# Optimization experiments

Hardware: AMD Instinct MI355X
Metric: run time of the kernel (lower is better)

## Reference

```python
import jax, jax.numpy as jnp
import numpy as np

N_NODES = 100000
N_EDGES = 3200000
DIM = 64


def setup_inputs() -> dict:
    key = jax.random.key(0)
    k1, k2, k3, k4, k5, k6 = jax.random.split(key, 6)
    lap_rows = jax.random.randint(k1, (N_EDGES,), 0, N_NODES, dtype=jnp.int32)
    lap_cols = jax.random.randint(k2, (N_EDGES,), 0, N_NODES, dtype=jnp.int32)
    # normalized-Laplacian-like positive values
    lap_vals = jax.random.uniform(k3, (N_EDGES,), dtype=jnp.float32) * 0.1
    features = jax.random.normal(k4, (N_NODES, DIM), dtype=jnp.float32)
    scale = 1.0 / np.sqrt(DIM)
    W1 = jax.random.normal(k5, (DIM, DIM), dtype=jnp.float32) * scale
    b1 = jnp.zeros((DIM,), dtype=jnp.float32)
    W2 = jax.random.normal(k6, (DIM, DIM), dtype=jnp.float32) * scale
    b2 = jnp.zeros((DIM,), dtype=jnp.float32)
    return {
        "lap_rows": lap_rows, "lap_cols": lap_cols, "lap_vals": lap_vals,
        "features": features, "W1": W1, "b1": b1, "W2": W2, "b2": b2,
    }


def reference(lap_rows, lap_cols, lap_vals, features, W1, b1, W2, b2):
    # x = L @ features  (COO SpMM: gather source rows, scale, scatter-add to dest)
    msgs = lap_vals[:, None] * features[lap_cols]            # [E, D]
    x = jax.ops.segment_sum(msgs, lap_rows, num_segments=N_NODES)  # [N, D]
    # output = (L+I) E W1 + (L E * E) W2
    inter_part1 = (features + x) @ W1 + b1                   # [N, D_out]
    inter_part2 = (x * features) @ W2 + b2                   # [N, D_out]
    return inter_part1 + inter_part2
```

## Files before the change

### kernel.cpp

```cpp
#include <hip/hip_runtime.h>
#include <hip/hip_fp16.h>

#define DIM 64
#define RPB 128
#define RPB_SHIFT 7
#define SUP_SHIFT 11
#define SB_MAX 64
#define HTILE_H 16384
#define HTILE1 4096
#define HTILE2 4096
#define XSCALE 4194304.0f
#define XINV   2.384185791015625e-7f

typedef _Float16 half8 __attribute__((ext_vector_type(8)));
typedef float    f32x4 __attribute__((ext_vector_type(4)));
typedef float    f32x2 __attribute__((ext_vector_type(2)));

template <bool HI>
__device__ __forceinline__ f32x2 q2f(unsigned int w)
{
    return __builtin_amdgcn_cvt_pk_f32_fp8(w, HI);
}

__global__ __launch_bounds__(256) void scatter_kernel(
    const int* __restrict__ rows, const int* __restrict__ cols,
    const float* __restrict__ vals, const float* __restrict__ feat,
    float* __restrict__ x, int E)
{
    unsigned long long t = (unsigned long long)blockIdx.x * blockDim.x + threadIdx.x;
    int e = (int)(t >> 6);
    int d = (int)(t & 63);
    if (e >= E) return;
    int r = rows[e];
    int c = cols[e];
    float v = vals[e];
    float f = feat[(size_t)c * DIM + d];
    atomicAdd(&x[(size_t)r * DIM + d], v * f);
}

__global__ __launch_bounds__(256) void cvt_kernel(
    const float* __restrict__ f, __half* __restrict__ h, int n2)
{
    int i = blockIdx.x * blockDim.x + threadIdx.x;
    if (i < n2) {
        float2 v = ((const float2*)f)[i];
        __half2 o;
        o.x = __float2half(v.x);
        o.y = __float2half(v.y);
        ((__half2*)h)[i] = o;
    }
}

__global__ __launch_bounds__(1024) void prep_kernel(
    const float* __restrict__ feat, __half* __restrict__ featH,
    unsigned char* __restrict__ featQ,
    const int* __restrict__ rows, int* __restrict__ gcnt,
    int n8, int NC, int E, int B)
{
    if ((int)blockIdx.x < NC) {
        int i = blockIdx.x * 1024 + threadIdx.x;
        if (i < n8) {
            const float4* src = (const float4*)(feat + (size_t)i * 8);
            float4 a = src[0], b = src[1];
            __half2 h0 = __floats2half2_rn(a.x, a.y);
            __half2 h1 = __floats2half2_rn(a.z, a.w);
            __half2 h2 = __floats2half2_rn(b.x, b.y);
            __half2 h3 = __floats2half2_rn(b.z, b.w);
            float4 ho;
            ho.x = __builtin_bit_cast(float, h0);
            ho.y = __builtin_bit_cast(float, h1);
            ho.z = __builtin_bit_cast(float, h2);
            ho.w = __builtin_bit_cast(float, h3);
            *(float4*)(featH + (size_t)i * 8) = ho;
            unsigned int q0 = __builtin_amdgcn_cvt_pk_fp8_f32(a.x, a.y, 0, false);
            q0 = __builtin_amdgcn_cvt_pk_fp8_f32(a.z, a.w, (int)q0, true);
            unsigned int q1 = __builtin_amdgcn_cvt_pk_fp8_f32(b.x, b.y, 0, false);
            q1 = __builtin_amdgcn_cvt_pk_fp8_f32(b.z, b.w, (int)q1, true);
            uint2 qo; qo.x = q0; qo.y = q1;
            *(uint2*)(featQ + (size_t)i * 8) = qo;
        }
    } else {
        extern __shared__ int lcnt[];
        for (int i = threadIdx.x; i < B; i += 1024) lcnt[i] = 0;
        __syncthreads();
        int base = ((int)blockIdx.x - NC) * HTILE_H;
#pragma unroll
        for (int k = 0; k < HTILE_H / 1024; ++k) {
            int e = base + k * 1024 + threadIdx.x;
            if (e < E) atomicAdd(&lcnt[rows[e] >> RPB_SHIFT], 1);
        }
        __syncthreads();
        for (int i = threadIdx.x; i < B; i += 1024)
            if (lcnt[i]) atomicAdd(&gcnt[i], lcnt[i]);
    }
}

__global__ __launch_bounds__(1024) void scan_kernel(
    const int* __restrict__ gcnt, int* __restrict__ offs, int* __restrict__ cursors,
    int* __restrict__ soffs, int* __restrict__ scursors, int B, int SB, int E)
{
    __shared__ int lds[2048];
    int t = threadIdx.x;
    int c0 = (t < B) ? gcnt[t] : 0;
    int c1 = (t + 1024 < B) ? gcnt[t + 1024] : 0;
    lds[t] = c0;
    lds[t + 1024] = c1;
    __syncthreads();
    for (int off = 1; off < 2048; off <<= 1) {
        int a = (t >= off) ? lds[t - off] : 0;
        int b = lds[t + 1024 - off];
        __syncthreads();
        lds[t] += a;
        lds[t + 1024] += b;
        __syncthreads();
    }
    if (t < B) {
        int e = lds[t] - c0;
        offs[t] = e; cursors[t] = e;
        if ((t & 15) == 0) { soffs[t >> 4] = e; scursors[t >> 4] = e; }
    }
    int t2 = t + 1024;
    if (t2 < B) {
        int e = lds[t2] - c1;
        offs[t2] = e; cursors[t2] = e;
        if ((t2 & 15) == 0) { soffs[t2 >> 4] = e; scursors[t2 >> 4] = e; }
    }
    if (t == 0) { offs[B] = E; soffs[SB] = E; }
}

__global__ __launch_bounds__(1024) void superbin_kernel(
    const int* __restrict__ rows, const int* __restrict__ cols,
    const float* __restrict__ vals, int* __restrict__ scursors,
    unsigned long long* __restrict__ sorted1, int E, int SB)
{
    __shared__ int cnt[SB_MAX];
    __shared__ int bse[SB_MAX];
    const int tid = threadIdx.x;
    if (tid < SB) cnt[tid] = 0;
    __syncthreads();
    const int tbase = blockIdx.x * HTILE1;
    int rr[HTILE1 / 1024];
#pragma unroll
    for (int k = 0; k < HTILE1 / 1024; ++k) {
        int e = tbase + k * 1024 + tid;
        rr[k] = (e < E) ? rows[e] : -1;
        if (rr[k] >= 0) atomicAdd(&cnt[rr[k] >> SUP_SHIFT], 1);
    }
    __syncthreads();
    if (tid < SB) {
        int c = cnt[tid];
        bse[tid] = c ? atomicAdd(&scursors[tid], c) : 0;
        cnt[tid] = 0;
    }
    __syncthreads();
#pragma unroll
    for (int k = 0; k < HTILE1 / 1024; ++k) {
        int e = tbase + k * 1024 + tid;
        if (rr[k] >= 0) {
            int r  = rr[k];
            int sb = r >> SUP_SHIFT;
            int slot = bse[sb] + atomicAdd(&cnt[sb], 1);
            unsigned long long pk =
                ((unsigned long long)__float_as_uint(vals[e]) << 32) |
                ((unsigned long long)(r & 2047) << 17) |
                (unsigned)cols[e];
            sorted1[slot] = pk;
        }
    }
}

__global__ __launch_bounds__(1024) void finebin_kernel(
    const unsigned long long* __restrict__ sorted1, const int* __restrict__ soffs,
    int* __restrict__ cursors, unsigned long long* __restrict__ sorted2,
    int E, int B, int SB)
{
    extern __shared__ int l[];
    int* cnt  = l;
    int* bse  = l + B;
    int* sofl = l + 2 * B;
    const int tid = threadIdx.x;
    if (tid <= SB) sofl[tid] = soffs[tid];
    for (int i = tid; i < B; i += 1024) cnt[i] = 0;
    __syncthreads();

    const int tbase = blockIdx.x * HTILE2;
    int sb0 = 0;
    {
        int lo = 0, hi = SB - 1;
        while (lo < hi) {
            int mid = (lo + hi + 1) >> 1;
            if (sofl[mid] <= tbase) lo = mid; else hi = mid - 1;
        }
        sb0 = lo;
    }

    unsigned long long pkr[HTILE2 / 1024];
    int fidr[HTILE2 / 1024];
#pragma unroll
    for (int k = 0; k < HTILE2 / 1024; ++k) {
        int i = tbase + k * 1024 + tid;
        if (i < E) {
            pkr[k] = sorted1[i];
            int sb = sb0;
            while (sofl[sb + 1] <= i) sb++;
            fidr[k] = (sb << 4) + (int)((pkr[k] >> 24) & 15);
            atomicAdd(&cnt[fidr[k]], 1);
        } else fidr[k] = -1;
    }
    __syncthreads();
    for (int i = tid; i < B; i += 1024) {
        int c = cnt[i];
        bse[i] = c ? atomicAdd(&cursors[i], c) : 0;
    }
    __syncthreads();
    for (int i = tid; i < B; i += 1024) cnt[i] = 0;
    __syncthreads();
#pragma unroll
    for (int k = 0; k < HTILE2 / 1024; ++k) {
        if (fidr[k] >= 0) {
            int f = fidr[k];
            int slot = bse[f] + atomicAdd(&cnt[f], 1);
            sorted2[slot] = pkr[k];
        }
    }
}

__global__ __launch_bounds__(1024, 4) void reduce_fused_mfma_kernel(
    const unsigned long long* __restrict__ sorted, const int* __restrict__ offs,
    const unsigned char* __restrict__ featQ, const __half* __restrict__ featH,
    const float* __restrict__ W1, const float* __restrict__ b1,
    const float* __restrict__ W2, const float* __restrict__ b2,
    float* __restrict__ out, int N)
{
    __shared__ int   xi[RPB][DIM + 4];
    __shared__ half8 Wl[1024];
    __shared__ float biasl[DIM];

    const int tid = threadIdx.x;
    const int b   = blockIdx.x;

    {
        int t    = tid >> 8;
        int c    = (tid >> 6) & 3;
        int quad = (tid >> 4) & 3;
        int m    = tid & 15;
        const float* Wsrc = (t < 2) ? W1 : W2;
        int kbase = (t & 1) * 32 + quad * 8;
        int col   = c * 16 + m;
        half8 wv;
#pragma unroll
        for (int j = 0; j < 8; ++j)
            wv[j] = (_Float16)Wsrc[(kbase + j) * DIM + col];
        Wl[tid] = wv;
        if (tid < DIM) biasl[tid] = b1[tid] + b2[tid];
    }
    for (int i = tid; i < RPB * (DIM + 4); i += 1024) ((int*)xi)[i] = 0;
    __syncthreads();

    const int s = offs[b], t = offs[b + 1];
    const int grp = tid >> 3;
    const int sub = tid & 7;
    const int rowbase = b * RPB;

#define EDGE_ACC(PK, Q)                                                      \
    {                                                                        \
        int   rl = (int)(((PK) >> 17) & (RPB - 1));                          \
        float v  = __uint_as_float((unsigned)((PK) >> 32)) * XSCALE;         \
        int* base = &xi[rl][sub * 8];                                        \
        f32x2 f0 = q2f<false>((Q).x);                                        \
        f32x2 f1 = q2f<true >((Q).x);                                        \
        f32x2 f2 = q2f<false>((Q).y);                                        \
        f32x2 f3 = q2f<true >((Q).y);                                        \
        atomicAdd(base + 0, (int)(f0[0] * v));                               \
        atomicAdd(base + 1, (int)(f0[1] * v));                               \
        atomicAdd(base + 2, (int)(f1[0] * v));                               \
        atomicAdd(base + 3, (int)(f1[1] * v));                               \
        atomicAdd(base + 4, (int)(f2[0] * v));                               \
        atomicAdd(base + 5, (int)(f2[1] * v));                               \
        atomicAdd(base + 6, (int)(f3[0] * v));                               \
        atomicAdd(base + 7, (int)(f3[1] * v));                               \
    }

    int i = s + grp;
    for (; i + 384 < t; i += 512) {
        unsigned long long pk0 = sorted[i];
        unsigned long long pk1 = sorted[i + 128];
        unsigned long long pk2 = sorted[i + 256];
        unsigned long long pk3 = sorted[i + 384];
        uint2 q0 = *(const uint2*)(featQ + ((size_t)(pk0 & 0x1FFFFu) << 6) + sub * 8);
        uint2 q1 = *(const uint2*)(featQ + ((size_t)(pk1 & 0x1FFFFu) << 6) + sub * 8);
        uint2 q2 = *(const uint2*)(featQ + ((size_t)(pk2 & 0x1FFFFu) << 6) + sub * 8);
        uint2 q3 = *(const uint2*)(featQ + ((size_t)(pk3 & 0x1FFFFu) << 6) + sub * 8);
        EDGE_ACC(pk0, q0)
        EDGE_ACC(pk1, q1)
        EDGE_ACC(pk2, q2)
        EDGE_ACC(pk3, q3)
    }
    for (; i < t; i += 128) {
        unsigned long long pk0 = sorted[i];
        uint2 q0 = *(const uint2*)(featQ + ((size_t)(pk0 & 0x1FFFFu) << 6) + sub * 8);
        EDGE_ACC(pk0, q0)
    }
#undef EDGE_ACC
    __syncthreads();

    const int w    = tid >> 6;
    const int lane = tid & 63;
    const int m    = lane & 15;
    const int quad = lane >> 4;

#pragma unroll
    for (int it = 0; it < 2; ++it) {
        int task = w + 16 * it;
        int tile = task >> 2;
        int cw   = task & 3;

        const int fb = cw * 64 + quad * 16 + m;
        half8 wf0 = Wl[fb];
        half8 wf1 = Wl[fb + 256];
        half8 wf2 = Wl[fb + 512];
        half8 wf3 = Wl[fb + 768];
        float bias = biasl[cw * 16 + m];

        int rowl = tile * 16 + m;
        int grow = rowbase + rowl;
        int rldr = (grow < N) ? grow : (N - 1);
        const __half* fp = featH + (size_t)rldr * DIM + quad * 8;
        half8 flo = *(const half8*)(fp);
        half8 fhi = *(const half8*)(fp + 32);
        const int* xp = &xi[rowl][quad * 8];
        int4 xl0 = *(const int4*)(xp);
        int4 xl1 = *(const int4*)(xp + 4);
        int4 xh0 = *(const int4*)(xp + 32);
        int4 xh1 = *(const int4*)(xp + 36);

        half8 alo, ahi, blo, bhi;
        _Float16 xv;
        xv = (_Float16)((float)xl0.x * XINV); alo[0] = flo[0] + xv; blo[0] = flo[0] * xv;
        xv = (_Float16)((float)xl0.y * XINV); alo[1] = flo[1] + xv; blo[1] = flo[1] * xv;
        xv = (_Float16)((float)xl0.z * XINV); alo[2] = flo[2] + xv; blo[2] = flo[2] * xv;
        xv = (_Float16)((float)xl0.w * XINV); alo[3] = flo[3] + xv; blo[3] = flo[3] * xv;
        xv = (_Float16)((float)xl1.x * XINV); alo[4] = flo[4] + xv; blo[4] = flo[4] * xv;
        xv = (_Float16)((float)xl1.y * XINV); alo[5] = flo[5] + xv; blo[5] = flo[5] * xv;
        xv = (_Float16)((float)xl1.z * XINV); alo[6] = flo[6] + xv; blo[6] = flo[6] * xv;
        xv = (_Float16)((float)xl1.w * XINV); alo[7] = flo[7] + xv; blo[7] = flo[7] * xv;
        xv = (_Float16)((float)xh0.x * XINV); ahi[0] = fhi[0] + xv; bhi[0] = fhi[0] * xv;
        xv = (_Float16)((float)xh0.y * XINV); ahi[1] = fhi[1] + xv; bhi[1] = fhi[1] * xv;
        xv = (_Float16)((float)xh0.z * XINV); ahi[2] = fhi[2] + xv; bhi[2] = fhi[2] * xv;
        xv = (_Float16)((float)xh0.w * XINV); ahi[3] = fhi[3] + xv; bhi[3] = fhi[3] * xv;
        xv = (_Float16)((float)xh1.x * XINV); ahi[4] = fhi[4] + xv; bhi[4] = fhi[4] * xv;
        xv = (_Float16)((float)xh1.y * XINV); ahi[5] = fhi[5] + xv; bhi[5] = fhi[5] * xv;
        xv = (_Float16)((float)xh1.z * XINV); ahi[6] = fhi[6] + xv; bhi[6] = fhi[6] * xv;
        xv = (_Float16)((float)xh1.w * XINV); ahi[7] = fhi[7] + xv; bhi[7] = fhi[7] * xv;

        f32x4 a0 = { bias, bias, bias, bias };
        a0 = __builtin_amdgcn_mfma_f32_16x16x32_f16(alo, wf0, a0, 0, 0, 0);
        a0 = __builtin_amdgcn_mfma_f32_16x16x32_f16(ahi, wf1, a0, 0, 0, 0);
        a0 = __builtin_amdgcn_mfma_f32_16x16x32_f16(blo, wf2, a0, 0, 0, 0);
        a0 = __builtin_amdgcn_mfma_f32_16x16x32_f16(bhi, wf3, a0, 0, 0, 0);

#pragma unroll
        for (int reg = 0; reg < 4; ++reg) {
            int orow = rowbase + tile * 16 + quad * 4 + reg;
            if (orow < N)
                out[(size_t)orow * DIM + cw * 16 + m] = a0[reg];
        }
    }
}

__global__ __launch_bounds__(256) void transform_mfma_kernel(
    const __half* __restrict__ featH, const float* __restrict__ x,
    const float* __restrict__ W1, const float* __restrict__ b1,
    const float* __restrict__ W2, const float* __restrict__ b2,
    float* __restrict__ out, int N)
{
    const int lane = threadIdx.x & 63;
    const int m    = lane & 15;
    const int quad = lane >> 4;

    half8 wfrag[4][4];
#pragma unroll
    for (int t = 0; t < 4; ++t) {
        const float* Wsrc = (t < 2) ? W1 : W2;
        int kbase = (t & 1) * 32 + quad * 8;
#pragma unroll
        for (int c = 0; c < 4; ++c) {
            int col = c * 16 + m;
            half8 w;
#pragma unroll
            for (int j = 0; j < 8; ++j)
                w[j] = (_Float16)Wsrc[(kbase + j) * DIM + col];
            wfrag[t][c] = w;
        }
    }
    float bias[4];
#pragma unroll
    for (int c = 0; c < 4; ++c)
        bias[c] = b1[c * 16 + m] + b2[c * 16 + m];

    const int ntiles = (N + 15) / 16;
    const int wid    = (int)((blockIdx.x * blockDim.x + threadIdx.x) >> 6);
    const int nwaves = (int)((gridDim.x * blockDim.x) >> 6);

    for (int tile = wid; tile < ntiles; tile += nwaves) {
        int row  = tile * 16 + m;
        int rldr = (row < N) ? row : (N - 1);
        const __half* fp = featH + (size_t)rldr * DIM + quad * 8;
        const float*  xp = x     + (size_t)rldr * DIM + quad * 8;
        half8 flo = *(const half8*)(fp);
        half8 fhi = *(const half8*)(fp + 32);
        float4 xl0 = *(const float4*)(xp);
        float4 xl1 = *(const float4*)(xp + 4);
        float4 xh0 = *(const float4*)(xp + 32);
        float4 xh1 = *(const float4*)(xp + 36);

        half8 alo, ahi, blo, bhi;
        _Float16 xv;
        xv = (_Float16)xl0.x; alo[0] = flo[0] + xv; blo[0] = flo[0] * xv;
        xv = (_Float16)xl0.y; alo[1] = flo[1] + xv; blo[1] = flo[1] * xv;
        xv = (_Float16)xl0.z; alo[2] = flo[2] + xv; blo[2] = flo[2] * xv;
        xv = (_Float16)xl0.w; alo[3] = flo[3] + xv; blo[3] = flo[3] * xv;
        xv = (_Float16)xl1.x; alo[4] = flo[4] + xv; blo[4] = flo[4] * xv;
        xv = (_Float16)xl1.y; alo[5] = flo[5] + xv; blo[5] = flo[5] * xv;
        xv = (_Float16)xl1.z; alo[6] = flo[6] + xv; blo[6] = flo[6] * xv;
        xv = (_Float16)xl1.w; alo[7] = flo[7] + xv; blo[7] = flo[7] * xv;
        xv = (_Float16)xh0.x; ahi[0] = fhi[0] + xv; bhi[0] = fhi[0] * xv;
        xv = (_Float16)xh0.y; ahi[1] = fhi[1] + xv; bhi[1] = fhi[1] * xv;
        xv = (_Float16)xh0.z; ahi[2] = fhi[2] + xv; bhi[2] = fhi[2] * xv;
        xv = (_Float16)xh0.w; ahi[3] = fhi[3] + xv; bhi[3] = fhi[3] * xv;
        xv = (_Float16)xh1.x; ahi[4] = fhi[4] + xv; bhi[4] = fhi[4] * xv;
        xv = (_Float16)xh1.y; ahi[5] = fhi[5] + xv; bhi[5] = fhi[5] * xv;
        xv = (_Float16)xh1.z; ahi[6] = fhi[6] + xv; bhi[6] = fhi[6] * xv;
        xv = (_Float16)xh1.w; ahi[7] = fhi[7] + xv; bhi[7] = fhi[7] * xv;

        f32x4 acc[4];
#pragma unroll
        for (int c = 0; c < 4; ++c) {
            f32x4 a0 = { bias[c], bias[c], bias[c], bias[c] };
            a0 = __builtin_amdgcn_mfma_f32_16x16x32_f16(alo, wfrag[0][c], a0, 0, 0, 0);
            a0 = __builtin_amdgcn_mfma_f32_16x16x32_f16(ahi, wfrag[1][c], a0, 0, 0, 0);
            a0 = __builtin_amdgcn_mfma_f32_16x16x32_f16(blo, wfrag[2][c], a0, 0, 0, 0);
            a0 = __builtin_amdgcn_mfma_f32_16x16x32_f16(bhi, wfrag[3][c], a0, 0, 0, 0);
            acc[c] = a0;
        }

#pragma unroll
        for (int reg = 0; reg < 4; ++reg) {
            int orow = tile * 16 + quad * 4 + reg;
            if (orow < N) {
#pragma unroll
                for (int c = 0; c < 4; ++c)
                    out[(size_t)orow * DIM + c * 16 + m] = acc[c][reg];
            }
        }
    }
}

extern "C" void kernel_launch(void* const* d_in, const int* in_sizes, int n_in,
                              void* d_out, int out_size, void* d_ws, size_t ws_size,
                              hipStream_t stream)
{
    const int*   rows = (const int*)d_in[0];
    const int*   cols = (const int*)d_in[1];
    const float* vals = (const float*)d_in[2];
    const float* feat = (const float*)d_in[3];
    const float* W1   = (const float*)d_in[4];
    const float* b1   = (const float*)d_in[5];
    const float* W2   = (const float*)d_in[6];
    const float* b2   = (const float*)d_in[7];
    float* out = (float*)d_out;

    const int E  = in_sizes[0];
    const int N  = in_sizes[3] / DIM;
    const int B  = (N + RPB - 1) / RPB;
    const int SB = (B + 15) / 16;

    char* ws = (char*)d_ws;
    size_t xBytes     = (size_t)N * DIM * sizeof(float);
    size_t hBytes     = (((size_t)N * DIM * sizeof(__half)) + 255) / 256 * 256;
    size_t qBytes     = (((size_t)N * DIM) + 255) / 256 * 256;
    size_t offsBytes  = (((size_t)(B + 1) * sizeof(int)) + 255) / 256 * 256;
    size_t cursBytes  = (((size_t)B * sizeof(int)) + 255) / 256 * 256;
    size_t soffBytes  = (((size_t)(SB + 1) * sizeof(int)) + 255) / 256 * 256;
    size_t scurBytes  = (((size_t)SB * sizeof(int)) + 255) / 256 * 256;
    size_t sortBytes  = (size_t)E * 8;

    float*              x        = (float*)ws;
    __half*             featH    = (__half*)(ws + xBytes);
    unsigned char*      featQ    = (unsigned char*)(ws + xBytes + hBytes);
    int*                offs     = (int*)(ws + xBytes + hBytes + qBytes);
    int*                cursors  = (int*)(ws + xBytes + hBytes + qBytes + offsBytes);
    int*                soffs    = (int*)(ws + xBytes + hBytes + qBytes + offsBytes + cursBytes);
    int*                scursors = (int*)(ws + xBytes + hBytes + qBytes + offsBytes + cursBytes + soffBytes);
    unsigned long long* sorted1  = (unsigned long long*)(ws + xBytes + hBytes + qBytes + offsBytes +
                                                         cursBytes + soffBytes + scurBytes);
    unsigned long long* sorted2  = sorted1 + E;
    size_t need = xBytes + hBytes + qBytes + offsBytes + cursBytes + soffBytes + scurBytes + 2 * sortBytes;

    if (ws_size >= need && B <= 2048 && SB <= SB_MAX && N <= 131072) {
        const int n8  = N * DIM / 8;
        const int NC  = (n8 + 1023) / 1024;
        const int NTH = (E + HTILE_H - 1) / HTILE_H;
        const int NT1 = (E + HTILE1 - 1) / HTILE1;
        const int NT2 = (E + HTILE2 - 1) / HTILE2;
        hipMemsetAsync(offs, 0, (size_t)(B + 1) * sizeof(int), stream);
        prep_kernel<<<NC + NTH, 1024, (size_t)B * 4, stream>>>(
            feat, featH, featQ, rows, offs, n8, NC, E, B);
        scan_kernel<<<1, 1024, 0, stream>>>(offs, offs, cursors, soffs, scursors, B, SB, E);
        superbin_kernel<<<NT1, 1024, 0, stream>>>(rows, cols, vals, scursors, sorted1, E, SB);
        finebin_kernel<<<NT2, 1024, (size_t)(2 * B + SB + 1) * 4, stream>>>(
            sorted1, soffs, cursors, sorted2, E, B, SB);
        reduce_fused_mfma_kernel<<<B, 1024, 0, stream>>>(sorted2, offs, featQ, featH,
                                                         W1, b1, W2, b2, out, N);
    } else {
        cvt_kernel<<<(N * DIM / 2 + 255) / 256, 256, 0, stream>>>(feat, featH, N * DIM / 2);
        hipMemsetAsync(x, 0, xBytes, stream);
        unsigned long long threads = (unsigned long long)E * DIM;
        unsigned int blocks = (unsigned int)((threads + 255ull) / 256ull);
        scatter_kernel<<<blocks, 256, 0, stream>>>(rows, cols, vals, feat, x, E);
        transform_mfma_kernel<<<640, 256, 0, stream>>>(featH, x, W1, b1, W2, b2, out, N);
    }
}
```

Measured before the change: 268.2 us.

## Halve rows per block, pad LDS stride to 65, unroll gather loop deeper

Reduces rows per reduce block from 128 to 64, which doubles the number of blocks and halves LDS use per block. Superbins are regrouped to 32 bins each so the superbin count stays within bounds. The LDS accumulator stride changes to 65 to spread atomic bank conflicts, the edge loop is unrolled to 8 gathers in flight with nontemporal loads of the sorted stream, and the MFMA epilogue becomes a single pass per wave. The trade-offs are more blocks each redoing the weight/LDS setup, and the padded stride stopping the vectorized int4 LDS reads in the epilogue.

```diff
diff --git a/kernel.cpp b/kernel.cpp
--- a/kernel.cpp
+++ b/kernel.cpp
@@ -2,10 +2,11 @@
 #include <hip/hip_fp16.h>
 
 #define DIM 64
-#define RPB 128
-#define RPB_SHIFT 7
+#define RPB 64
+#define RPB_SHIFT 6
 #define SUP_SHIFT 11
 #define SB_MAX 64
+#define XSTRIDE 65
 #define HTILE_H 16384
 #define HTILE1 4096
 #define HTILE2 4096
@@ -117,13 +118,13 @@
     if (t < B) {
         int e = lds[t] - c0;
         offs[t] = e; cursors[t] = e;
-        if ((t & 15) == 0) { soffs[t >> 4] = e; scursors[t >> 4] = e; }
+        if ((t & 31) == 0) { soffs[t >> 5] = e; scursors[t >> 5] = e; }
     }
     int t2 = t + 1024;
     if (t2 < B) {
         int e = lds[t2] - c1;
         offs[t2] = e; cursors[t2] = e;
-        if ((t2 & 15) == 0) { soffs[t2 >> 4] = e; scursors[t2 >> 4] = e; }
+        if ((t2 & 31) == 0) { soffs[t2 >> 5] = e; scursors[t2 >> 5] = e; }
     }
     if (t == 0) { offs[B] = E; soffs[SB] = E; }
 }
@@ -203,7 +204,7 @@
             pkr[k] = sorted1[i];
             int sb = sb0;
             while (sofl[sb + 1] <= i) sb++;
-            fidr[k] = (sb << 4) + (int)((pkr[k] >> 24) & 15);
+            fidr[k] = (sb << 5) + (int)((pkr[k] >> 23) & 31);
             atomicAdd(&cnt[fidr[k]], 1);
         } else fidr[k] = -1;
     }
@@ -232,7 +233,7 @@
     const float* __restrict__ W2, const float* __restrict__ b2,
     float* __restrict__ out, int N)
 {
-    __shared__ int   xi[RPB][DIM + 4];
+    __shared__ int   xi[RPB * XSTRIDE];
     __shared__ half8 Wl[1024];
     __shared__ float biasl[DIM];
 
@@ -254,7 +255,7 @@
         Wl[tid] = wv;
         if (tid < DIM) biasl[tid] = b1[tid] + b2[tid];
     }
-    for (int i = tid; i < RPB * (DIM + 4); i += 1024) ((int*)xi)[i] = 0;
+    for (int i = tid; i < RPB * XSTRIDE; i += 1024) xi[i] = 0;
     __syncthreads();
 
     const int s = offs[b], t = offs[b + 1];
@@ -266,7 +267,7 @@
     {                                                                        \
         int   rl = (int)(((PK) >> 17) & (RPB - 1));                          \
         float v  = __uint_as_float((unsigned)((PK) >> 32)) * XSCALE;         \
-        int* base = &xi[rl][sub * 8];                                        \
+        int* base = &xi[rl * XSTRIDE + sub * 8];                             \
         f32x2 f0 = q2f<false>((Q).x);                                        \
         f32x2 f1 = q2f<true >((Q).x);                                        \
         f32x2 f2 = q2f<false>((Q).y);                                        \
@@ -280,27 +281,55 @@
         atomicAdd(base + 6, (int)(f3[0] * v));                               \
         atomicAdd(base + 7, (int)(f3[1] * v));                               \
     }
+#define GATHER(PK) (*(const uint2*)(featQ + ((size_t)((PK) & 0x1FFFFu) << 6) + sub * 8))
 
     int i = s + grp;
-    for (; i + 384 < t; i += 512) {
-        unsigned long long pk0 = sorted[i];
-        unsigned long long pk1 = sorted[i + 128];
-        unsigned long long pk2 = sorted[i + 256];
-        unsigned long long pk3 = sorted[i + 384];
-        uint2 q0 = *(const uint2*)(featQ + ((size_t)(pk0 & 0x1FFFFu) << 6) + sub * 8);
-        uint2 q1 = *(const uint2*)(featQ + ((size_t)(pk1 & 0x1FFFFu) << 6) + sub * 8);
-        uint2 q2 = *(const uint2*)(featQ + ((size_t)(pk2 & 0x1FFFFu) << 6) + sub * 8);
-        uint2 q3 = *(const uint2*)(featQ + ((size_t)(pk3 & 0x1FFFFu) << 6) + sub * 8);
+    for (; i + 896 < t; i += 1024) {
+        unsigned long long pk0 = __builtin_nontemporal_load(sorted + i);
+        unsigned long long pk1 = __builtin_nontemporal_load(sorted + i + 128);
+        unsigned long long pk2 = __builtin_nontemporal_load(sorted + i + 256);
+        unsigned long long pk3 = __builtin_nontemporal_load(sorted + i + 384);
+        unsigned long long pk4 = __builtin_nontemporal_load(sorted + i + 512);
+        unsigned long long pk5 = __builtin_nontemporal_load(sorted + i + 640);
+        unsigned long long pk6 = __builtin_nontemporal_load(sorted + i + 768);
+        unsigned long long pk7 = __builtin_nontemporal_load(sorted + i + 896);
+        uint2 q0 = GATHER(pk0);
+        uint2 q1 = GATHER(pk1);
+        uint2 q2 = GATHER(pk2);
+        uint2 q3 = GATHER(pk3);
+        uint2 q4 = GATHER(pk4);
+        uint2 q5 = GATHER(pk5);
+        uint2 q6 = GATHER(pk6);
+        uint2 q7 = GATHER(pk7);
         EDGE_ACC(pk0, q0)
         EDGE_ACC(pk1, q1)
         EDGE_ACC(pk2, q2)
         EDGE_ACC(pk3, q3)
+        EDGE_ACC(pk4, q4)
+        EDGE_ACC(pk5, q5)
+        EDGE_ACC(pk6, q6)
+        EDGE_ACC(pk7, q7)
+    }
+    for (; i + 384 < t; i += 512) {
+        unsigned long long pk0 = __builtin_nontemporal_load(sorted + i);
+        unsigned long long pk1 = __builtin_nontemporal_load(sorted + i + 128);
+        unsigned long long pk2 = __builtin_nontemporal_load(sorted + i + 256);
+        unsigned long long pk3 = __builtin_nontemporal_load(sorted + i + 384);
+        uint2 q0 = GATHER(pk0);
+        uint2 q1 = GATHER(pk1);
+        uint2 q2 = GATHER(pk2);
+        uint2 q3 = GATHER(pk3);
+        EDGE_ACC(pk0, q0)
+        EDGE_ACC(pk1, q1)
+        EDGE_ACC(pk2, q2)
+        EDGE_ACC(pk3, q3)
     }
     for (; i < t; i += 128) {
-        unsigned long long pk0 = sorted[i];
-        uint2 q0 = *(const uint2*)(featQ + ((size_t)(pk0 & 0x1FFFFu) << 6) + sub * 8);
+        unsigned long long pk0 = __builtin_nontemporal_load(sorted + i);
+        uint2 q0 = GATHER(pk0);
         EDGE_ACC(pk0, q0)
     }
+#undef GATHER
 #undef EDGE_ACC
     __syncthreads();
 
@@ -308,63 +337,54 @@
     const int lane = tid & 63;
     const int m    = lane & 15;
     const int quad = lane >> 4;
-
-#pragma unroll
-    for (int it = 0; it < 2; ++it) {
-        int task = w + 16 * it;
-        int tile = task >> 2;
-        int cw   = task & 3;
-
-        const int fb = cw * 64 + quad * 16 + m;
-        half8 wf0 = Wl[fb];
-        half8 wf1 = Wl[fb + 256];
-        half8 wf2 = Wl[fb + 512];
-        half8 wf3 = Wl[fb + 768];
-        float bias = biasl[cw * 16 + m];
-
-        int rowl = tile * 16 + m;
-        int grow = rowbase + rowl;
-        int rldr = (grow < N) ? grow : (N - 1);
-        const __half* fp = featH + (size_t)rldr * DIM + quad * 8;
-        half8 flo = *(const half8*)(fp);
-        half8 fhi = *(const half8*)(fp + 32);
-        const int* xp = &xi[rowl][quad * 8];
-        int4 xl0 = *(const int4*)(xp);
-        int4 xl1 = *(const int4*)(xp + 4);
-        int4 xh0 = *(const int4*)(xp + 32);
-        int4 xh1 = *(const int4*)(xp + 36);
-
-        half8 alo, ahi, blo, bhi;
-        _Float16 xv;
-        xv = (_Float16)((float)xl0.x * XINV); alo[0] = flo[0] + xv; blo[0] = flo[0] * xv;
-        xv = (_Float16)((float)xl0.y * XINV); alo[1] = flo[1] + xv; blo[1] = flo[1] * xv;
-        xv = (_Float16)((float)xl0.z * XINV); alo[2] = flo[2] + xv; blo[2] = flo[2] * xv;
-        xv = (_Float16)((float)xl0.w * XINV); alo[3] = flo[3] + xv; blo[3] = flo[3] * xv;
-        xv = (_Float16)((float)xl1.x * XINV); alo[4] = flo[4] + xv; blo[4] = flo[4] * xv;
-        xv = (_Float16)((float)xl1.y * XINV); alo[5] = flo[5] + xv; blo[5] = flo[5] * xv;
-        xv = (_Float16)((float)xl1.z * XINV); alo[6] = flo[6] + xv; blo[6] = flo[6] * xv;
-        xv = (_Float16)((float)xl1.w * XINV); alo[7] = flo[7] + xv; blo[7] = flo[7] * xv;
-        xv = (_Float16)((float)xh0.x * XINV); ahi[0] = fhi[0] + xv; bhi[0] = fhi[0] * xv;
-        xv = (_Float16)((float)xh0.y * XINV); ahi[1] = fhi[1] + xv; bhi[1] = fhi[1] * xv;
-        xv = (_Float16)((float)xh0.z * XINV); ahi[2] = fhi[2] + xv; bhi[2] = fhi[2] * xv;
-        xv = (_Float16)((float)xh0.w * XINV); ahi[3] = fhi[3] + xv; bhi[3] = fhi[3] * xv;
-        xv = (_Float16)((float)xh1.x * XINV); ahi[4] = fhi[4] + xv; bhi[4] = fhi[4] * xv;
-        xv = (_Float16)((float)xh1.y * XINV); ahi[5] = fhi[5] + xv; bhi[5] = fhi[5] * xv;
-        xv = (_Float16)((float)xh1.z * XINV); ahi[6] = fhi[6] + xv; bhi[6] = fhi[6] * xv;
-        xv = (_Float16)((float)xh1.w * XINV); ahi[7] = fhi[7] + xv; bhi[7] = fhi[7] * xv;
-
-        f32x4 a0 = { bias, bias, bias, bias };
-        a0 = __builtin_amdgcn_mfma_f32_16x16x32_f16(alo, wf0, a0, 0, 0, 0);
-        a0 = __builtin_amdgcn_mfma_f32_16x16x32_f16(ahi, wf1, a0, 0, 0, 0);
-        a0 = __builtin_amdgcn_mfma_f32_16x16x32_f16(blo, wf2, a0, 0, 0, 0);
-        a0 = __builtin_amdgcn_mfma_f32_16x16x32_f16(bhi, wf3, a0, 0, 0, 0);
-
-#pragma unroll
-        for (int reg = 0; reg < 4; ++reg) {
-            int orow = rowbase + tile * 16 + quad * 4 + reg;
-            if (orow < N)
-                out[(size_t)orow * DIM + cw * 16 + m] = a0[reg];
-        }
+    const int tile = w >> 2;
+    const int cw   = w & 3;
+
+    const int fb = cw * 64 + quad * 16 + m;
+    half8 wf0 = Wl[fb];
+    half8 wf1 = Wl[fb + 256];
+    half8 wf2 = Wl[fb + 512];
+    half8 wf3 = Wl[fb + 768];
+    float bias = biasl[cw * 16 + m];
+
+    int rowl = tile * 16 + m;
+    int grow = rowbase + rowl;
+    int rldr = (grow < N) ? grow : (N - 1);
+    const __half* fp = featH + (size_t)rldr * DIM + quad * 8;
+    half8 flo = *(const half8*)(fp);
+    half8 fhi = *(const half8*)(fp + 32);
+    const int* xp = &xi[rowl * XSTRIDE + quad * 8];
+
+    half8 alo, ahi, blo, bhi;
+    _Float16 xv;
+    xv = (_Float16)((float)xp[0] * XINV);  alo[0] = flo[0] + xv; blo[0] = flo[0] * xv;
+    xv = (_Float16)((float)xp[1] * XINV);  alo[1] = flo[1] + xv; blo[1] = flo[1] * xv;
+    xv = (_Float16)((float)xp[2] * XINV);  alo[2] = flo[2] + xv; blo[2] = flo[2] * xv;
+    xv = (_Float16)((float)xp[3] * XINV);  alo[3] = flo[3] + xv; blo[3] = flo[3] * xv;
+    xv = (_Float16)((float)xp[4] * XINV);  alo[4] = flo[4] + xv; blo[4] = flo[4] * xv;
+    xv = (_Float16)((float)xp[5] * XINV);  alo[5] = flo[5] + xv; blo[5] = flo[5] * xv;
+    xv = (_Float16)((float)xp[6] * XINV);  alo[6] = flo[6] + xv; blo[6] = flo[6] * xv;
+    xv = (_Float16)((float)xp[7] * XINV);  alo[7] = flo[7] + xv; blo[7] = flo[7] * xv;
+    xv = (_Float16)((float)xp[32] * XINV); ahi[0] = fhi[0] + xv; bhi[0] = fhi[0] * xv;
+    xv = (_Float16)((float)xp[33] * XINV); ahi[1] = fhi[1] + xv; bhi[1] = fhi[1] * xv;
+    xv = (_Float16)((float)xp[34] * XINV); ahi[2] = fhi[2] + xv; bhi[2] = fhi[2] * xv;
+    xv = (_Float16)((float)xp[35] * XINV); ahi[3] = fhi[3] + xv; bhi[3] = fhi[3] * xv;
+    xv = (_Float16)((float)xp[36] * XINV); ahi[4] = fhi[4] + xv; bhi[4] = fhi[4] * xv;
+    xv = (_Float16)((float)xp[37] * XINV); ahi[5] = fhi[5] + xv; bhi[5] = fhi[5] * xv;
+    xv = (_Float16)((float)xp[38] * XINV); ahi[6] = fhi[6] + xv; bhi[6] = fhi[6] * xv;
+    xv = (_Float16)((float)xp[39] * XINV); ahi[7] = fhi[7] + xv; bhi[7] = fhi[7] * xv;
+
+    f32x4 a0 = { bias, bias, bias, bias };
+    a0 = __builtin_amdgcn_mfma_f32_16x16x32_f16(alo, wf0, a0, 0, 0, 0);
+    a0 = __builtin_amdgcn_mfma_f32_16x16x32_f16(ahi, wf1, a0, 0, 0, 0);
+    a0 = __builtin_amdgcn_mfma_f32_16x16x32_f16(blo, wf2, a0, 0, 0, 0);
+    a0 = __builtin_amdgcn_mfma_f32_16x16x32_f16(bhi, wf3, a0, 0, 0, 0);
+
+#pragma unroll
+    for (int reg = 0; reg < 4; ++reg) {
+        int orow = rowbase + tile * 16 + quad * 4 + reg;
+        if (orow < N)
+            out[(size_t)orow * DIM + cw * 16 + m] = a0[reg];
     }
 }
 
@@ -473,7 +493,7 @@
     const int E  = in_sizes[0];
     const int N  = in_sizes[3] / DIM;
     const int B  = (N + RPB - 1) / RPB;
-    const int SB = (B + 15) / 16;
+    const int SB = (B + 31) / 32;
 
     char* ws = (char*)d_ws;
     size_t xBytes     = (size_t)N * DIM * sizeof(float);
```

New measurement: 262.1 us. 2.3% less time.
